# Kernel tuning notes

Hardware: AMD Instinct MI355X
Metric: run time of the kernel (lower is better)

The kernel has to match this reference:

```python
import jax, jax.numpy as jnp
import numpy as np

DIM = 512
DIM_HEAD = 32
HEADS = DIM // DIM_HEAD
WS = 8  # window (partition) size
INNER = (DIM * 4 * 2 // 3 // 32) * 32  # gated-MLP inner dim = 2720
EPS = 1e-6
LS_INIT = 1e-5


def _ln(x, g, b):
    mu = jnp.mean(x, axis=-1, keepdims=True)
    var = jnp.var(x, axis=-1, keepdims=True)
    return (x - mu) * jax.lax.rsqrt(var + EPS) * g + b


def setup_inputs() -> dict:
    key = jax.random.key(0)
    ks = jax.random.split(key, 8)
    B, H, W = 8, 96, 96
    s = lambda d: 1.0 / np.sqrt(d)
    return {
        "x": jax.random.normal(ks[0], (B, H, W, DIM), jnp.float32),
        "norm1_g": jnp.ones((DIM,), jnp.float32),
        "norm1_b": jnp.zeros((DIM,), jnp.float32),
        "qkv_w": jax.random.normal(ks[1], (DIM, 3 * DIM), jnp.float32) * s(DIM),
        "qkv_b": jnp.zeros((3 * DIM,), jnp.float32),
        "proj_w": jax.random.normal(ks[2], (DIM, DIM), jnp.float32) * s(DIM),
        "proj_b": jnp.zeros((DIM,), jnp.float32),
        "ls1": jnp.full((DIM,), LS_INIT, jnp.float32),
        "norm2_g": jnp.ones((DIM,), jnp.float32),
        "norm2_b": jnp.zeros((DIM,), jnp.float32),
        "glu_w": jax.random.normal(ks[3], (DIM, 2 * INNER), jnp.float32) * s(DIM),
        "glu_b": jnp.zeros((2 * INNER,), jnp.float32),
        "fc2_w": jax.random.normal(ks[4], (INNER, DIM), jnp.float32) * s(INNER),
        "fc2_b": jnp.zeros((DIM,), jnp.float32),
        "ls2": jnp.full((DIM,), LS_INIT, jnp.float32),
    }


def reference(x, norm1_g, norm1_b, qkv_w, qkv_b, proj_w, proj_b, ls1,
              norm2_g, norm2_b, glu_w, glu_b, fc2_w, fc2_b, ls2):
    B, H, W, C = x.shape
    nH, nW = H // WS, W // WS
    T = WS * WS  # tokens per window

    # ---- window attention branch ----
    y = _ln(x, norm1_g, norm1_b)
    # window_partition: (B,H,W,C) -> (B*nH*nW, T, C)
    y = y.reshape(B, nH, WS, nW, WS, C).transpose(0, 1, 3, 2, 4, 5)
    y = y.reshape(-1, T, C)
    qkv = y @ qkv_w + qkv_b                      # (M, T, 3C)
    qkv = qkv.reshape(-1, T, 3, HEADS, DIM_HEAD)
    q, k, v = qkv[:, :, 0], qkv[:, :, 1], qkv[:, :, 2]   # (M, T, h, d)
    scale = DIM_HEAD ** -0.5
    attn = jnp.einsum('mqhd,mkhd->mhqk', q, k) * scale
    attn = jax.nn.softmax(attn, axis=-1)
    o = jnp.einsum('mhqk,mkhd->mqhd', attn, v).reshape(-1, T, C)
    o = o @ proj_w + proj_b
    # window_reverse: (M, T, C) -> (B, H, W, C)
    o = o.reshape(B, nH, nW, WS, WS, C).transpose(0, 1, 3, 2, 4, 5)
    o = o.reshape(B, H, W, C)
    x = x + ls1 * o

    # ---- gated MLP branch (GLU with SiLU) ----
    y = _ln(x, norm2_g, norm2_b)
    h = y @ glu_w + glu_b
    h, gate = jnp.split(h, 2, axis=-1)
    h = h * jax.nn.silu(gate)
    h = h @ fc2_w + fc2_b
    x = x + ls2 * h
    return x
```

## Files before the change

kernel.cpp:

```cpp
#include <hip/hip_runtime.h>
#include <hip/hip_bf16.h>
#include <stdint.h>

#define DIM 512
#define INNER 1344
#define INNERP 1408

typedef __attribute__((ext_vector_type(8))) short vbf8;
typedef __attribute__((ext_vector_type(4))) float vf4;
typedef __attribute__((ext_vector_type(2))) float vf2;
typedef __attribute__((ext_vector_type(4))) int v4i;
typedef __attribute__((ext_vector_type(8))) int v8i;

typedef __attribute__((address_space(1))) void as1void;
typedef __attribute__((address_space(3))) void as3void;

union frag8 {
  v8i w;
  v4i h[2];
};

__device__ __forceinline__ unsigned pk4fp8(float a, float b, float c, float d) {
  int v = __builtin_amdgcn_cvt_pk_fp8_f32(a, b, 0, false);
  v = __builtin_amdgcn_cvt_pk_fp8_f32(c, d, v, true);
  return (unsigned)v;
}
__device__ __forceinline__ uint8_t q8(float v) {
  return (uint8_t)(__builtin_amdgcn_cvt_pk_fp8_f32(v, v, 0, false) & 0xff);
}
__device__ __forceinline__ vbf8 cvt8fp8(uint2 wv) {
  union {
    vbf8 v;
    __hip_bfloat16 e[8];
  } o;
  vf2 f;
  f = __builtin_amdgcn_cvt_pk_f32_fp8((int)wv.x, false);
  o.e[0] = __float2bfloat16(f.x);
  o.e[1] = __float2bfloat16(f.y);
  f = __builtin_amdgcn_cvt_pk_f32_fp8((int)wv.x, true);
  o.e[2] = __float2bfloat16(f.x);
  o.e[3] = __float2bfloat16(f.y);
  f = __builtin_amdgcn_cvt_pk_f32_fp8((int)wv.y, false);
  o.e[4] = __float2bfloat16(f.x);
  o.e[5] = __float2bfloat16(f.y);
  f = __builtin_amdgcn_cvt_pk_f32_fp8((int)wv.y, true);
  o.e[6] = __float2bfloat16(f.x);
  o.e[7] = __float2bfloat16(f.y);
  return o.v;
}

#define MFMA_SC(a, b, c) \
  __builtin_amdgcn_mfma_scale_f32_16x16x128_f8f6f4((a), (b), (c), 0, 0, 0, 127, 0, 127)

__global__ void k_transpose(const float* __restrict__ Wsrc, uint8_t* __restrict__ WT,
                            int K, int N, int ldOut, int nsplit) {
  __shared__ float tile[32][33];
  const int tx = threadIdx.x, ty = threadIdx.y;
  const int n0 = blockIdx.x * 32, k0 = blockIdx.y * 32;
#pragma unroll
  for (int i = 0; i < 32; i += 8) {
    int k = k0 + ty + i, n = n0 + tx;
    if (k < K && n < N) tile[ty + i][tx] = Wsrc[(size_t)k * N + n];
  }
  __syncthreads();
#pragma unroll
  for (int i = 0; i < 32; i += 8) {
    int n = n0 + ty + i, k = k0 + tx;
    if (n < N && k < K) {
      int np = n + (n >= nsplit ? 64 : 0);
      WT[(size_t)np * ldOut + k] = q8(tile[tx][ty + i]);
    }
  }
}

__global__ void k_padbias(const float* __restrict__ b, float* __restrict__ o) {
  int c = blockIdx.x * 256 + threadIdx.x;
  if (c < INNER) o[c] = b[c];
  else if (c >= INNERP && c < INNERP + INNER) o[c] = b[c - 64];
  else if (c < 2816) o[c] = 0.0f;
}

template <bool PART, bool BF16IN>
__global__ __launch_bounds__(256) void k_ln(const void* __restrict__ xin,
                                            const float* __restrict__ gw,
                                            const float* __restrict__ bw,
                                            uint8_t* __restrict__ y) {
  const int wave = threadIdx.x >> 6, lane = threadIdx.x & 63;
  const int tok = blockIdx.x * 4 + wave;
  float vals[8];
  if (BF16IN) {
    const __hip_bfloat16* xr = (const __hip_bfloat16*)xin + (size_t)tok * DIM + lane * 8;
    union {
      vbf8 v;
      ushort e[8];
    } u;
    u.v = *(const vbf8*)xr;
#pragma unroll
    for (int j = 0; j < 8; ++j) vals[j] = __uint_as_float((unsigned)u.e[j] << 16);
  } else {
    const float* xr = (const float*)xin + (size_t)tok * DIM + lane * 8;
    const float4 v0 = *(const float4*)xr;
    const float4 v1 = *(const float4*)(xr + 4);
    vals[0] = v0.x; vals[1] = v0.y; vals[2] = v0.z; vals[3] = v0.w;
    vals[4] = v1.x; vals[5] = v1.y; vals[6] = v1.z; vals[7] = v1.w;
  }
  float s = 0.f, ss = 0.f;
#pragma unroll
  for (int j = 0; j < 8; ++j) {
    s += vals[j];
    ss += vals[j] * vals[j];
  }
#pragma unroll
  for (int off = 32; off > 0; off >>= 1) {
    s += __shfl_xor(s, off);
    ss += __shfl_xor(ss, off);
  }
  const float mu = s * (1.0f / DIM);
  const float rs = rsqrtf(ss * (1.0f / DIM) - mu * mu + 1e-6f);
  size_t orow;
  if (PART) {
    int b = tok / 9216, rem = tok % 9216;
    int h = rem / 96, w = rem % 96;
    orow = (size_t)(((b * 12 + (h >> 3)) * 12 + (w >> 3)) * 64 + (h & 7) * 8 + (w & 7));
  } else {
    orow = (size_t)tok;
  }
  const float4 g0 = *(const float4*)(gw + lane * 8);
  const float4 g1 = *(const float4*)(gw + lane * 8 + 4);
  const float4 b0 = *(const float4*)(bw + lane * 8);
  const float4 b1 = *(const float4*)(bw + lane * 8 + 4);
  const float gg[8] = {g0.x, g0.y, g0.z, g0.w, g1.x, g1.y, g1.z, g1.w};
  const float bb[8] = {b0.x, b0.y, b0.z, b0.w, b1.x, b1.y, b1.z, b1.w};
  float r[8];
#pragma unroll
  for (int j = 0; j < 8; ++j) r[j] = (vals[j] - mu) * rs * gg[j] + bb[j];
  uint2 po;
  po.x = pk4fp8(r[0], r[1], r[2], r[3]);
  po.y = pk4fp8(r[4], r[5], r[6], r[7]);
  *(uint2*)(y + orow * DIM + lane * 8) = po;
}

template <int K, int MODE, int NT>
__global__ __launch_bounds__(256, 2) void k_gemm128(const uint8_t* __restrict__ A8,
                                                    const uint8_t* __restrict__ W8,
                                                    const float* __restrict__ bias,
                                                    void* __restrict__ outp,
                                                    const void* __restrict__ resid,
                                                    const float* __restrict__ lsv,
                                                    const int ldOut) {
  __shared__ alignas(16) char As[128 * 128];
  __shared__ alignas(16) char Ws[128 * 128];
  const int nwg = gridDim.x;
  int bid = blockIdx.x;
  bid = (bid & 7) * (nwg >> 3) + (bid >> 3);
  const int bm = bid / NT, bn = bid % NT;
  const int tid = threadIdx.x, wave = tid >> 6, lane = tid & 63;
  const int wr = wave >> 1, wc = wave & 1;
  const int cl = lane & 15, g = lane >> 4;
  constexpr int nkt = K >> 7;

  const int r0 = wave * 32;
  const int ro = lane >> 3, pb = lane & 7;
  const int swz = (pb ^ ro) << 4;
  const uint8_t* asrc = A8 + (size_t)bm * 128 * K + (size_t)(r0 + ro) * K + swz;
  const uint8_t* wsrc = W8 + (size_t)bn * 128 * K + (size_t)(r0 + ro) * K + swz;
  char* adst = As + r0 * 128;
  char* wdst = Ws + r0 * 128;

  int aoff[4][2], woff[4][2];
#pragma unroll
  for (int i = 0; i < 4; ++i) {
    const int ra = wr * 64 + cl + i * 16;
    const int rb = wc * 64 + cl + i * 16;
    aoff[i][0] = ra * 128 + (((2 * g) ^ (ra & 7)) << 4);
    aoff[i][1] = ra * 128 + (((2 * g + 1) ^ (ra & 7)) << 4);
    woff[i][0] = rb * 128 + (((2 * g) ^ (rb & 7)) << 4);
    woff[i][1] = rb * 128 + (((2 * g + 1) ^ (rb & 7)) << 4);
  }

  vf4 acc[4][4] = {};

  for (int t = 0; t < nkt; ++t) {
    __syncthreads();
#pragma unroll
    for (int c = 0; c < 32; c += 8) {
      __builtin_amdgcn_global_load_lds((const as1void*)(asrc + (size_t)c * K),
                                       (as3void*)(adst + c * 128), 16, 0, 0);
      __builtin_amdgcn_global_load_lds((const as1void*)(wsrc + (size_t)c * K),
                                       (as3void*)(wdst + c * 128), 16, 0, 0);
    }
    asrc += 128;
    wsrc += 128;
    __syncthreads();
    frag8 af[4], wf[4];
#pragma unroll
    for (int i = 0; i < 4; ++i) {
      af[i].h[0] = *(const v4i*)(As + aoff[i][0]);
      af[i].h[1] = *(const v4i*)(As + aoff[i][1]);
      wf[i].h[0] = *(const v4i*)(Ws + woff[i][0]);
      wf[i].h[1] = *(const v4i*)(Ws + woff[i][1]);
    }
#pragma unroll
    for (int mi = 0; mi < 4; ++mi)
#pragma unroll
      for (int ni = 0; ni < 4; ++ni)
        acc[mi][ni] = MFMA_SC(af[mi].w, wf[ni].w, acc[mi][ni]);
  }

  const int rl = g << 2;
  const int rbase = bm * 128 + wr * 64;
  const int cbase = bn * 128 + wc * 64;
#pragma unroll
  for (int mi = 0; mi < 4; ++mi) {
#pragma unroll
    for (int j = 0; j < 4; ++j) {
      const int r = rbase + mi * 16 + rl + j;
      size_t orow;
      if (MODE == 1) {
        int m = r >> 6, t2 = r & 63;
        int b = m / 144, mm = m % 144;
        int wh = mm / 12, ww = mm % 12;
        int h = wh * 8 + (t2 >> 3), w = ww * 8 + (t2 & 7);
        orow = (size_t)((b * 96 + h) * 96 + w);
      } else {
        orow = (size_t)r;
      }
#pragma unroll
      for (int ni = 0; ni < 4; ++ni) {
        const int c = cbase + ni * 16 + cl;
        const float v = acc[mi][ni][j] + bias[c];
        if (MODE == 0) {
          ((uint8_t*)outp)[(size_t)r * ldOut + c] = q8(v);
        } else if (MODE == 1) {
          const float* rx = (const float*)resid;
          ((__hip_bfloat16*)outp)[orow * DIM + c] =
              __float2bfloat16(rx[orow * DIM + c] + lsv[c] * v);
        } else {
          const __hip_bfloat16* rx = (const __hip_bfloat16*)resid;
          ((float*)outp)[(size_t)r * DIM + c] =
              __bfloat162float(rx[(size_t)r * DIM + c]) + lsv[c] * v;
        }
      }
    }
  }
}

__global__ __launch_bounds__(256, 2) void k_gemm_glu(const uint8_t* __restrict__ A8,
                                                     const uint8_t* __restrict__ W8,
                                                     const float* __restrict__ bias,
                                                     uint8_t* __restrict__ hout) {
  __shared__ alignas(16) char As[128 * 128];
  __shared__ alignas(16) char B0s[64 * 128];
  __shared__ alignas(16) char B1s[64 * 128];
  constexpr int K = DIM;
  const int nwg = gridDim.x;
  int bid = blockIdx.x;
  bid = (bid & 7) * (nwg >> 3) + (bid >> 3);
  const int bm = bid / 22, bn = bid % 22;
  const int tid = threadIdx.x, wave = tid >> 6, lane = tid & 63;
  const int wr = wave >> 1, wc = wave & 1;
  const int cl = lane & 15, g = lane >> 4;

  const int ro = lane >> 3, pb = lane & 7;
  const int swz = (pb ^ ro) << 4;
  const int r0a = wave * 32, r0b = wave * 16;
  const uint8_t* asrc = A8 + (size_t)bm * 128 * K + (size_t)(r0a + ro) * K + swz;
  const uint8_t* b0src = W8 + (size_t)(bn * 64 + r0b + ro) * K + swz;
  const uint8_t* b1src = W8 + (size_t)(INNERP + bn * 64 + r0b + ro) * K + swz;
  char* adst = As + r0a * 128;
  char* b0dst = B0s + r0b * 128;
  char* b1dst = B1s + r0b * 128;

  int aoff[4][2], boff[2][2];
#pragma unroll
  for (int i = 0; i < 4; ++i) {
    const int ra = wr * 64 + cl + i * 16;
    aoff[i][0] = ra * 128 + (((2 * g) ^ (ra & 7)) << 4);
    aoff[i][1] = ra * 128 + (((2 * g + 1) ^ (ra & 7)) << 4);
  }
#pragma unroll
  for (int i = 0; i < 2; ++i) {
    const int rb = wc * 32 + cl + i * 16;
    boff[i][0] = rb * 128 + (((2 * g) ^ (rb & 7)) << 4);
    boff[i][1] = rb * 128 + (((2 * g + 1) ^ (rb & 7)) << 4);
  }

  vf4 a0[4][2] = {}, a1[4][2] = {};

#pragma unroll
  for (int t = 0; t < 4; ++t) {
    __syncthreads();
#pragma unroll
    for (int c = 0; c < 32; c += 8)
      __builtin_amdgcn_global_load_lds((const as1void*)(asrc + (size_t)c * K),
                                       (as3void*)(adst + c * 128), 16, 0, 0);
#pragma unroll
    for (int c = 0; c < 16; c += 8) {
      __builtin_amdgcn_global_load_lds((const as1void*)(b0src + (size_t)c * K),
                                       (as3void*)(b0dst + c * 128), 16, 0, 0);
      __builtin_amdgcn_global_load_lds((const as1void*)(b1src + (size_t)c * K),
                                       (as3void*)(b1dst + c * 128), 16, 0, 0);
    }
    asrc += 128;
    b0src += 128;
    b1src += 128;
    __syncthreads();
    frag8 af[4], w0f[2], w1f[2];
#pragma unroll
    for (int i = 0; i < 4; ++i) {
      af[i].h[0] = *(const v4i*)(As + aoff[i][0]);
      af[i].h[1] = *(const v4i*)(As + aoff[i][1]);
    }
#pragma unroll
    for (int i = 0; i < 2; ++i) {
      w0f[i].h[0] = *(const v4i*)(B0s + boff[i][0]);
      w0f[i].h[1] = *(const v4i*)(B0s + boff[i][1]);
      w1f[i].h[0] = *(const v4i*)(B1s + boff[i][0]);
      w1f[i].h[1] = *(const v4i*)(B1s + boff[i][1]);
    }
#pragma unroll
    for (int mi = 0; mi < 4; ++mi)
#pragma unroll
      for (int ni = 0; ni < 2; ++ni) {
        a0[mi][ni] = MFMA_SC(af[mi].w, w0f[ni].w, a0[mi][ni]);
        a1[mi][ni] = MFMA_SC(af[mi].w, w1f[ni].w, a1[mi][ni]);
      }
  }

  const int rl = g << 2;
  const int rbase = bm * 128 + wr * 64;
  const int cbase = bn * 64 + wc * 32;
#pragma unroll
  for (int mi = 0; mi < 4; ++mi)
#pragma unroll
    for (int j = 0; j < 4; ++j) {
      const int r = rbase + mi * 16 + rl + j;
#pragma unroll
      for (int ni = 0; ni < 2; ++ni) {
        const int c = cbase + ni * 16 + cl;
        const float a = a0[mi][ni][j] + bias[c];
        const float gv = a1[mi][ni][j] + bias[INNERP + c];
        const float sg = 1.0f / (1.0f + __expf(-gv));
        hout[(size_t)r * INNERP + c] = q8(a * gv * sg);
      }
    }
}

__global__ __launch_bounds__(256, 2) void k_attn_mfma(const uint8_t* __restrict__ qkv,
                                                      uint8_t* __restrict__ o) {
  __shared__ __hip_bfloat16 sm[4][6912];
  const int wave = threadIdx.x >> 6, lane = threadIdx.x & 63;
  const int task = blockIdx.x * 4 + wave;
  const int w = task >> 4, hd = task & 15;
  const int g = lane >> 4, c = lane & 15;
  __hip_bfloat16* smp = sm[wave];
  __hip_bfloat16* smv = smp + 4608;

  const uint8_t* base = qkv + (size_t)w * 64 * 1536 + hd * 32;

  vbf8 qf[4], kf[4];
#pragma unroll
  for (int i = 0; i < 4; ++i) {
    const uint8_t* qrow = base + (size_t)(i * 16 + c) * 1536 + g * 8;
    qf[i] = cvt8fp8(*(const uint2*)qrow);
    kf[i] = cvt8fp8(*(const uint2*)(qrow + 512));
  }

  {
    const uint8_t* vrow = base + (size_t)lane * 1536 + 1024;
    union {
      vbf8 v;
      ushort e[8];
    } uv;
#pragma unroll
    for (int i = 0; i < 4; ++i) {
      uv.v = cvt8fp8(*(const uint2*)(vrow + i * 8));
#pragma unroll
      for (int j = 0; j < 8; ++j)
        ((ushort*)smv)[(i * 8 + j) * 72 + lane] = uv.e[j];
    }
  }

  vf4 st[4][4];
#pragma unroll
  for (int iq = 0; iq < 4; ++iq)
#pragma unroll
    for (int it = 0; it < 4; ++it) {
      vf4 z = {};
      st[iq][it] = __builtin_amdgcn_mfma_f32_16x16x32_bf16(qf[iq], kf[it], z, 0, 0, 0);
    }

  float inv[4][4];
#pragma unroll
  for (int iq = 0; iq < 4; ++iq) {
#pragma unroll
    for (int j = 0; j < 4; ++j) {
      float m = fmaxf(fmaxf(st[iq][0][j], st[iq][1][j]), fmaxf(st[iq][2][j], st[iq][3][j]));
      m = fmaxf(m, __shfl_xor(m, 1));
      m = fmaxf(m, __shfl_xor(m, 2));
      m = fmaxf(m, __shfl_xor(m, 4));
      m = fmaxf(m, __shfl_xor(m, 8));
      float s = 0.f;
#pragma unroll
      for (int it = 0; it < 4; ++it) {
        const float e = __expf((st[iq][it][j] - m) * 0.17677669529663687f);
        st[iq][it][j] = e;
        s += e;
      }
      s += __shfl_xor(s, 1);
      s += __shfl_xor(s, 2);
      s += __shfl_xor(s, 4);
      s += __shfl_xor(s, 8);
      inv[iq][j] = 1.0f / s;
    }
  }

#pragma unroll
  for (int iq = 0; iq < 4; ++iq)
#pragma unroll
    for (int j = 0; j < 4; ++j) {
      const int q = iq * 16 + g * 4 + j;
#pragma unroll
      for (int it = 0; it < 4; ++it)
        smp[q * 72 + it * 16 + c] = __float2bfloat16(st[iq][it][j]);
    }

  vf4 ot[4][2] = {};
#pragma unroll
  for (int ks = 0; ks < 2; ++ks) {
    vbf8 pf[4], vfr[2];
#pragma unroll
    for (int iq = 0; iq < 4; ++iq)
      pf[iq] = *(const vbf8*)(smp + (iq * 16 + c) * 72 + ks * 32 + g * 8);
#pragma unroll
    for (int dt = 0; dt < 2; ++dt)
      vfr[dt] = *(const vbf8*)(smv + (dt * 16 + c) * 72 + ks * 32 + g * 8);
#pragma unroll
    for (int iq = 0; iq < 4; ++iq)
#pragma unroll
      for (int dt = 0; dt < 2; ++dt)
        ot[iq][dt] = __builtin_amdgcn_mfma_f32_16x16x32_bf16(pf[iq], vfr[dt], ot[iq][dt], 0, 0, 0);
  }

#pragma unroll
  for (int iq = 0; iq < 4; ++iq)
#pragma unroll
    for (int dt = 0; dt < 2; ++dt)
#pragma unroll
      for (int j = 0; j < 4; ++j) {
        const int q = iq * 16 + g * 4 + j;
        smp[q * 72 + dt * 16 + c] = __float2bfloat16(ot[iq][dt][j] * inv[iq][j]);
      }
  uint8_t* ob = o + (size_t)w * 64 * 512 + hd * 32;
#pragma unroll
  for (int i = 0; i < 4; ++i) {
    const int idx = i * 64 + lane;
    const int row = idx >> 2, chunk = idx & 3;
    union {
      vbf8 v;
      ushort e[8];
    } u;
    u.v = *(const vbf8*)(smp + row * 72 + chunk * 8);
    float f[8];
#pragma unroll
    for (int j = 0; j < 8; ++j) f[j] = __uint_as_float((unsigned)u.e[j] << 16);
    uint2 pv;
    pv.x = pk4fp8(f[0], f[1], f[2], f[3]);
    pv.y = pk4fp8(f[4], f[5], f[6], f[7]);
    *(uint2*)(ob + (size_t)row * 512 + chunk * 8) = pv;
  }
}

extern "C" void kernel_launch(void* const* d_in, const int* in_sizes, int n_in, void* d_out,
                              int out_size, void* d_ws, size_t ws_size, hipStream_t stream) {
  const float* x = (const float*)d_in[0];
  const float* n1g = (const float*)d_in[1];
  const float* n1b = (const float*)d_in[2];
  const float* qkv_w = (const float*)d_in[3];
  const float* qkv_b = (const float*)d_in[4];
  const float* proj_w = (const float*)d_in[5];
  const float* proj_b = (const float*)d_in[6];
  const float* ls1 = (const float*)d_in[7];
  const float* n2g = (const float*)d_in[8];
  const float* n2b = (const float*)d_in[9];
  const float* glu_w = (const float*)d_in[10];
  const float* glu_b = (const float*)d_in[11];
  const float* fc2_w = (const float*)d_in[12];
  const float* fc2_b = (const float*)d_in[13];
  const float* ls2 = (const float*)d_in[14];

  if (ws_size < 268000000u) return;

  char* ws = (char*)d_ws;
  uint8_t* wTq = (uint8_t*)(ws + 0);
  uint8_t* wTp = (uint8_t*)(ws + 786432);
  uint8_t* wTg = (uint8_t*)(ws + 1048576);
  uint8_t* wTf = (uint8_t*)(ws + 2490368);
  float* gbias = (float*)(ws + 3211264);
  uint8_t* act8 = (uint8_t*)(ws + 3222528);
  char* big = ws + 40971264;
  uint8_t* qkv8 = (uint8_t*)big;
  uint8_t* h8 = (uint8_t*)big;
  __hip_bfloat16* x1b = (__hip_bfloat16*)(big + 113246208);

  hipMemsetAsync(wTg, 0, 1441792, stream);
  hipMemsetAsync(wTf, 0, 720896, stream);

  dim3 tb(32, 8);
  k_transpose<<<dim3(48, 16), tb, 0, stream>>>(qkv_w, wTq, 512, 1536, 512, 1 << 30);
  k_transpose<<<dim3(16, 16), tb, 0, stream>>>(proj_w, wTp, 512, 512, 512, 1 << 30);
  k_transpose<<<dim3(84, 16), tb, 0, stream>>>(glu_w, wTg, 512, 2688, 512, INNER);
  k_transpose<<<dim3(16, 42), tb, 0, stream>>>(fc2_w, wTf, 1344, 512, 1408, 1 << 30);
  k_padbias<<<11, 256, 0, stream>>>(glu_b, gbias);

  k_ln<true, false><<<18432, 256, 0, stream>>>(x, n1g, n1b, act8);
  k_gemm128<512, 0, 12><<<6912, 256, 0, stream>>>(act8, wTq, qkv_b, qkv8, nullptr, nullptr, 1536);
  k_attn_mfma<<<4608, 256, 0, stream>>>(qkv8, act8);
  k_gemm128<512, 1, 4><<<2304, 256, 0, stream>>>(act8, wTp, proj_b, (void*)x1b, x, ls1, 512);
  k_ln<false, true><<<18432, 256, 0, stream>>>(x1b, n2g, n2b, act8);
  k_gemm_glu<<<12672, 256, 0, stream>>>(act8, wTg, gbias, h8);
  k_gemm128<1408, 2, 4><<<2304, 256, 0, stream>>>(h8, wTf, fc2_b, d_out, x1b, ls2, 512);
}
```

Baseline: 541.4 us.

## Enlarge GEMM tiles to 256 rows with 512-thread blocks

```diff
diff --git a/kernel.cpp b/kernel.cpp
--- a/kernel.cpp
+++ b/kernel.cpp
@@ -141,14 +141,14 @@
 }
 
 template <int K, int MODE, int NT>
-__global__ __launch_bounds__(256, 2) void k_gemm128(const uint8_t* __restrict__ A8,
+__global__ __launch_bounds__(512, 4) void k_gemm256(const uint8_t* __restrict__ A8,
                                                     const uint8_t* __restrict__ W8,
                                                     const float* __restrict__ bias,
                                                     void* __restrict__ outp,
                                                     const void* __restrict__ resid,
                                                     const float* __restrict__ lsv,
                                                     const int ldOut) {
-  __shared__ alignas(16) char As[128 * 128];
+  __shared__ alignas(16) char As[256 * 128];
   __shared__ alignas(16) char Ws[128 * 128];
   const int nwg = gridDim.x;
   int bid = blockIdx.x;
@@ -159,13 +159,14 @@
   const int cl = lane & 15, g = lane >> 4;
   constexpr int nkt = K >> 7;
 
-  const int r0 = wave * 32;
   const int ro = lane >> 3, pb = lane & 7;
   const int swz = (pb ^ ro) << 4;
-  const uint8_t* asrc = A8 + (size_t)bm * 128 * K + (size_t)(r0 + ro) * K + swz;
-  const uint8_t* wsrc = W8 + (size_t)bn * 128 * K + (size_t)(r0 + ro) * K + swz;
-  char* adst = As + r0 * 128;
-  char* wdst = Ws + r0 * 128;
+  const int r0a = wave * 32;
+  const int r0w = wave * 16;
+  const uint8_t* asrc = A8 + (size_t)bm * 256 * K + (size_t)(r0a + ro) * K + swz;
+  const uint8_t* wsrc = W8 + (size_t)bn * 128 * K + (size_t)(r0w + ro) * K + swz;
+  char* adst = As + r0a * 128;
+  char* wdst = Ws + r0w * 128;
 
   int aoff[4][2], woff[4][2];
 #pragma unroll
@@ -183,12 +184,13 @@
   for (int t = 0; t < nkt; ++t) {
     __syncthreads();
 #pragma unroll
-    for (int c = 0; c < 32; c += 8) {
+    for (int c = 0; c < 32; c += 8)
       __builtin_amdgcn_global_load_lds((const as1void*)(asrc + (size_t)c * K),
                                        (as3void*)(adst + c * 128), 16, 0, 0);
+#pragma unroll
+    for (int c = 0; c < 16; c += 8)
       __builtin_amdgcn_global_load_lds((const as1void*)(wsrc + (size_t)c * K),
                                        (as3void*)(wdst + c * 128), 16, 0, 0);
-    }
     asrc += 128;
     wsrc += 128;
     __syncthreads();
@@ -208,7 +210,7 @@
   }
 
   const int rl = g << 2;
-  const int rbase = bm * 128 + wr * 64;
+  const int rbase = bm * 256 + wr * 64;
   const int cbase = bn * 128 + wc * 64;
 #pragma unroll
   for (int mi = 0; mi < 4; ++mi) {
@@ -245,11 +247,11 @@
   }
 }
 
-__global__ __launch_bounds__(256, 2) void k_gemm_glu(const uint8_t* __restrict__ A8,
+__global__ __launch_bounds__(512, 4) void k_gemm_glu(const uint8_t* __restrict__ A8,
                                                      const uint8_t* __restrict__ W8,
                                                      const float* __restrict__ bias,
                                                      uint8_t* __restrict__ hout) {
-  __shared__ alignas(16) char As[128 * 128];
+  __shared__ alignas(16) char As[256 * 128];
   __shared__ alignas(16) char B0s[64 * 128];
   __shared__ alignas(16) char B1s[64 * 128];
   constexpr int K = DIM;
@@ -263,8 +265,8 @@
 
   const int ro = lane >> 3, pb = lane & 7;
   const int swz = (pb ^ ro) << 4;
-  const int r0a = wave * 32, r0b = wave * 16;
-  const uint8_t* asrc = A8 + (size_t)bm * 128 * K + (size_t)(r0a + ro) * K + swz;
+  const int r0a = wave * 32, r0b = wave * 8;
+  const uint8_t* asrc = A8 + (size_t)bm * 256 * K + (size_t)(r0a + ro) * K + swz;
   const uint8_t* b0src = W8 + (size_t)(bn * 64 + r0b + ro) * K + swz;
   const uint8_t* b1src = W8 + (size_t)(INNERP + bn * 64 + r0b + ro) * K + swz;
   char* adst = As + r0a * 128;
@@ -294,13 +296,8 @@
     for (int c = 0; c < 32; c += 8)
       __builtin_amdgcn_global_load_lds((const as1void*)(asrc + (size_t)c * K),
                                        (as3void*)(adst + c * 128), 16, 0, 0);
-#pragma unroll
-    for (int c = 0; c < 16; c += 8) {
-      __builtin_amdgcn_global_load_lds((const as1void*)(b0src + (size_t)c * K),
-                                       (as3void*)(b0dst + c * 128), 16, 0, 0);
-      __builtin_amdgcn_global_load_lds((const as1void*)(b1src + (size_t)c * K),
-                                       (as3void*)(b1dst + c * 128), 16, 0, 0);
-    }
+    __builtin_amdgcn_global_load_lds((const as1void*)b0src, (as3void*)b0dst, 16, 0, 0);
+    __builtin_amdgcn_global_load_lds((const as1void*)b1src, (as3void*)b1dst, 16, 0, 0);
     asrc += 128;
     b0src += 128;
     b1src += 128;
@@ -328,7 +325,7 @@
   }
 
   const int rl = g << 2;
-  const int rbase = bm * 128 + wr * 64;
+  const int rbase = bm * 256 + wr * 64;
   const int cbase = bn * 64 + wc * 32;
 #pragma unroll
   for (int mi = 0; mi < 4; ++mi)
@@ -514,10 +511,10 @@
   k_padbias<<<11, 256, 0, stream>>>(glu_b, gbias);
 
   k_ln<true, false><<<18432, 256, 0, stream>>>(x, n1g, n1b, act8);
-  k_gemm128<512, 0, 12><<<6912, 256, 0, stream>>>(act8, wTq, qkv_b, qkv8, nullptr, nullptr, 1536);
+  k_gemm256<512, 0, 12><<<3456, 512, 0, stream>>>(act8, wTq, qkv_b, qkv8, nullptr, nullptr, 1536);
   k_attn_mfma<<<4608, 256, 0, stream>>>(qkv8, act8);
-  k_gemm128<512, 1, 4><<<2304, 256, 0, stream>>>(act8, wTp, proj_b, (void*)x1b, x, ls1, 512);
+  k_gemm256<512, 1, 4><<<1152, 512, 0, stream>>>(act8, wTp, proj_b, (void*)x1b, x, ls1, 512);
   k_ln<false, true><<<18432, 256, 0, stream>>>(x1b, n2g, n2b, act8);
-  k_gemm_glu<<<12672, 256, 0, stream>>>(act8, wTg, gbias, h8);
-  k_gemm128<1408, 2, 4><<<2304, 256, 0, stream>>>(h8, wTf, fc2_b, d_out, x1b, ls2, 512);
-}
+  k_gemm_glu<<<6336, 512, 0, stream>>>(act8, wTg, gbias, h8);
+  k_gemm256<1408, 2, 4><<<1152, 512, 0, stream>>>(h8, wTf, fc2_b, d_out, x1b, ls2, 512);
+}
```

Result: slower. 673.6 us (+24.4%).
